# Kernel optimization log

Measured on AMD Instinct MI355X. Metric: run time of the kernel, lower is better.

The kernel has to match this reference:

```python
import jax, jax.numpy as jnp
import numpy as np

NUM_EMBEDDINGS = 1024
EMBEDDING_DIM = 256
COMMITMENT_COST = 0.25
B, C, T = 16, 256, 4096


def setup_inputs() -> dict:
    key = jax.random.key(0)
    k_in, k_cb = jax.random.split(key)
    inputs = jax.random.normal(k_in, (B, C, T), dtype=jnp.float32)
    # matches nn.Embedding init uniform_(-1/K, 1/K)
    codebook = jax.random.uniform(
        k_cb, (NUM_EMBEDDINGS, EMBEDDING_DIM), dtype=jnp.float32,
        minval=-1.0 / NUM_EMBEDDINGS, maxval=1.0 / NUM_EMBEDDINGS)
    return {"inputs": inputs, "codebook": codebook}


def reference(inputs, codebook):
    # inputs: [B, C, T] -> [B, T, C] (channel-last), eval mode (no dead-code swap)
    x = jnp.transpose(inputs, (0, 2, 1))            # [B, T, C]
    flat = x.reshape(-1, EMBEDDING_DIM)             # [N, D]
    distances = (jnp.sum(flat * flat, axis=1, keepdims=True)
                 + jnp.sum(codebook * codebook, axis=1)
                 - 2.0 * jnp.matmul(flat, codebook.T))   # [N, K]
    encoding_indices = jnp.argmin(distances, axis=1)     # [N]
    quantized = codebook[encoding_indices].reshape(x.shape)  # [B, T, C]
    sg = jax.lax.stop_gradient
    e_latent_loss = jnp.mean(jnp.square(sg(quantized) - x))
    q_latent_loss = jnp.mean(jnp.square(quantized - sg(x)))
    vq_loss = e_latent_loss + COMMITMENT_COST * q_latent_loss
    quantized_st = x + sg(quantized - x)                 # straight-through
    quantized_st = jnp.transpose(quantized_st, (0, 2, 1))  # back to [B, C, T]
    indices = encoding_indices.reshape(B, T)
    return quantized_st, vq_loss, indices
```

## Files before the change

kernel.cpp:

```cpp
#include <hip/hip_runtime.h>
#include <stdint.h>

#define DIMS 256
#define NT 4096
#define NROWS 65536
#define THETA 1.5e-4f

typedef float    f32x4_t __attribute__((ext_vector_type(4)));
typedef _Float16 f16x8_t __attribute__((ext_vector_type(8)));
typedef _Float16 f16x4_t __attribute__((ext_vector_type(4)));

__global__ __launch_bounds__(64) void vq_prep(const float* __restrict__ cb,
                                              float* __restrict__ se,
                                              _Float16* __restrict__ cb16){
  __shared__ float sq[256];
  const int k = blockIdx.x;
  const int tid = threadIdx.x;
  float4 v = *(const float4*)(cb + (size_t)k*256 + tid*4);
  f16x4_t p;
  p.x = (_Float16)(v.x * 512.f);
  p.y = (_Float16)(v.y * 512.f);
  p.z = (_Float16)(v.z * 512.f);
  p.w = (_Float16)(v.w * 512.f);
  *(f16x4_t*)(cb16 + (size_t)k*256 + tid*4) = p;
  sq[tid*4+0] = __fmul_rn(v.x, v.x);
  sq[tid*4+1] = __fmul_rn(v.y, v.y);
  sq[tid*4+2] = __fmul_rn(v.z, v.z);
  sq[tid*4+3] = __fmul_rn(v.w, v.w);
  __syncthreads();
  if (tid < 16){
    const int h = tid >> 3, j = tid & 7;
    float r = sq[h*128 + j];
    #pragma unroll
    for (int i = 1; i < 16; ++i) r = __fadd_rn(r, sq[h*128 + j + 8*i]);
    r = __fadd_rn(r, __shfl_xor(r, 1));
    r = __fadd_rn(r, __shfl_xor(r, 2));
    r = __fadd_rn(r, __shfl_xor(r, 4));
    r = __fadd_rn(r, __shfl_xor(r, 8));
    if (tid == 0) se[k] = r;
  }
}


#define AH(r,c)    Ah[(size_t)(r)*264 + (c)]
#define BHL(s,k,c) Bh[((size_t)((s)*256 + (k)))*40 + (c)]
#define QQ(t,c)    q[(size_t)(t)*260 + (c)]

#define T2I(v, i, v1, i1, v2) { \
  bool lt = (v) < (v1); \
  (v2) = lt ? (v1) : fminf((v2), (v)); \
  (i1) = lt ? (i) : (i1); \
  (v1) = lt ? (v) : (v1); }

#define DECL_T2(M,R) \
  float b1_##M##R = 3.4e38f, b2_##M##R = 3.4e38f; int bi_##M##R = 0x7fffffff;

#define FOLD(M,R) { \
  float v; \
  v = fmaf(a##M##0[R], NEGI, ec0); T2I(v, kb +  0, b1_##M##R, bi_##M##R, b2_##M##R); \
  v = fmaf(a##M##1[R], NEGI, ec1); T2I(v, kb + 16, b1_##M##R, bi_##M##R, b2_##M##R); \
  v = fmaf(a##M##2[R], NEGI, ec2); T2I(v, kb + 32, b1_##M##R, bi_##M##R, b2_##M##R); \
  v = fmaf(a##M##3[R], NEGI, ec3); T2I(v, kb + 48, b1_##M##R, bi_##M##R, b2_##M##R); }

#define BSTEP(CC, S) { \
  *(f16x8_t*)&BHL((CC)&1, codeS, cOff)     = rb##S##0; \
  *(f16x8_t*)&BHL((CC)&1, codeS, cOff + 8) = rb##S##1; \
  asm volatile("s_waitcnt lgkmcnt(0)" ::: "memory"); \
  __builtin_amdgcn_s_barrier(); \
  asm volatile("" ::: "memory"); \
  { \
    const int nn = ktb + (CC) + 2; \
    if (nn < 32){ \
      const _Float16* p_ = cb16 + ((size_t)((nn>>3)*256) + codeS)*DIMS + (nn&7)*32 + cOff; \
      rb##S##0 = *(const f16x8_t*)(p_); rb##S##1 = *(const f16x8_t*)(p_ + 8); \
    } \
  } \
  { \
    f16x8_t bh0 = *(const f16x8_t*)&BHL((CC)&1, bC0, fq8); \
    f16x8_t bh1 = *(const f16x8_t*)&BHL((CC)&1, bC1, fq8); \
    f16x8_t bh2 = *(const f16x8_t*)&BHL((CC)&1, bC2, fq8); \
    f16x8_t bh3 = *(const f16x8_t*)&BHL((CC)&1, bC3, fq8); \
    f16x8_t ah0 = *(const f16x8_t*)&AH(wr32 + fr, (CC)*32 + fq8); \
    f16x8_t ah1 = *(const f16x8_t*)&AH(wr32 + 16 + fr, (CC)*32 + fq8); \
    a00 = __builtin_amdgcn_mfma_f32_16x16x32_f16(ah0, bh0, a00, 0, 0, 0); \
    a01 = __builtin_amdgcn_mfma_f32_16x16x32_f16(ah0, bh1, a01, 0, 0, 0); \
    a02 = __builtin_amdgcn_mfma_f32_16x16x32_f16(ah0, bh2, a02, 0, 0, 0); \
    a03 = __builtin_amdgcn_mfma_f32_16x16x32_f16(ah0, bh3, a03, 0, 0, 0); \
    a10 = __builtin_amdgcn_mfma_f32_16x16x32_f16(ah1, bh0, a10, 0, 0, 0); \
    a11 = __builtin_amdgcn_mfma_f32_16x16x32_f16(ah1, bh1, a11, 0, 0, 0); \
    a12 = __builtin_amdgcn_mfma_f32_16x16x32_f16(ah1, bh2, a12, 0, 0, 0); \
    a13 = __builtin_amdgcn_mfma_f32_16x16x32_f16(ah1, bh3, a13, 0, 0, 0); \
  } }

#define MSTEP(MK) { \
  float ov1 = __shfl_xor(v1, MK); int oi1 = __shfl_xor(i1, MK); float ov2 = __shfl_xor(v2, MK); \
  bool tk = ov1 < v1; \
  v2 = tk ? fminf(v1, ov2) : fminf(v2, ov1); \
  i1 = tk ? oi1 : i1; \
  v1 = tk ? ov1 : v1; }

#define MERGE(M,R) { \
  float v1 = b1_##M##R, v2 = b2_##M##R; int i1 = bi_##M##R; \
  MSTEP(1) MSTEP(2) MSTEP(4) MSTEP(8) \
  if (fr == 0) comb[(wr32 + (M)*16 + fq*4 + (R))*4 + wc] = make_float4(v1, __int_as_float(i1), v2, 0.f); }

__global__ __launch_bounds__(512, 1) void vq_scores(
    const float* __restrict__ x, const float* __restrict__ cb,
    const _Float16* __restrict__ cb16, const float* __restrict__ se,
    float* __restrict__ out0, float* __restrict__ out2,
    unsigned* __restrict__ wl, unsigned* __restrict__ cnt, double* __restrict__ accd)
{
  __shared__ __align__(16) char smem[79360];
  _Float16* Ah   = (_Float16*)smem;
  _Float16* Bh   = (_Float16*)(smem + 33792);
  float4*   comb = (float4*)(smem + 74752);
  int*      codeL= (int*)(smem + 78848);
  float*    sxa  = (float*)(smem + 79104);
  float*    q    = (float*)smem;

  const int tid  = threadIdx.x;
  const int lane = tid & 63;
  const int wid  = tid >> 6;
  const int wr   = wid >> 2;
  const int wc   = wid & 3;
  const int fr   = lane & 15;
  const int fq   = lane >> 4;
  const int wr32 = wr * 32;
  const int fq8  = fq * 8;
  const int wcfr = wc*64 + fr;
  const int n0   = blockIdx.x * 64;
  const int bb   = n0 >> 12;
  const int t0   = n0 & 4095;
  const float NEGI = -1.0f/256.0f;

  const int codeS = tid >> 1;
  const int cOff  = (tid & 1) << 4;

  f16x8_t rbA0, rbA1, rbB0, rbB1;
  {
    const _Float16* p_ = cb16 + (size_t)codeS * DIMS + cOff;
    rbA0 = *(const f16x8_t*)(p_); rbA1 = *(const f16x8_t*)(p_ + 8);
  }
  {
    const _Float16* p_ = cb16 + (size_t)codeS * DIMS + 32 + cOff;
    rbB0 = *(const f16x8_t*)(p_); rbB1 = *(const f16x8_t*)(p_ + 8);
  }

  {
    const int dup = tid >> 7;
    const int c4  = tid & 7;
    const int tt  = ((tid >> 3) & 15) << 2;
    #pragma unroll
    for (int cc2 = 0; cc2 < 2; ++cc2){
      const int c0 = (dup*2 + cc2) * 32;
      const float* xp = x + ((size_t)(bb*DIMS + c0 + c4*4))*NT + t0 + tt;
      float4 va0 = *(const float4*)(xp);
      float4 va1 = *(const float4*)(xp + NT);
      float4 va2 = *(const float4*)(xp + 2*NT);
      float4 va3 = *(const float4*)(xp + 3*NT);
      #pragma unroll
      for (int j = 0; j < 4; ++j){
        f16x4_t p;
        p.x = (_Float16)((&va0.x)[j]);
        p.y = (_Float16)((&va1.x)[j]);
        p.z = (_Float16)((&va2.x)[j]);
        p.w = (_Float16)((&va3.x)[j]);
        *(f16x4_t*)&AH(tt + j, c0 + c4*4) = p;
      }
    }
  }

  const f32x4_t Z = {0.f, 0.f, 0.f, 0.f};
  f32x4_t a00=Z,a01=Z,a02=Z,a03=Z, a10=Z,a11=Z,a12=Z,a13=Z;
  DECL_T2(0,0) DECL_T2(0,1) DECL_T2(0,2) DECL_T2(0,3)
  DECL_T2(1,0) DECL_T2(1,1) DECL_T2(1,2) DECL_T2(1,3)

  const int bC0 = wc*64 + 0*16 + fr;
  const int bC1 = wc*64 + 1*16 + fr;
  const int bC2 = wc*64 + 2*16 + fr;
  const int bC3 = wc*64 + 3*16 + fr;

  for (int kt = 0; kt < 4; ++kt){
    const int ktb = kt * 8;
    BSTEP(0,A) BSTEP(1,B) BSTEP(2,A) BSTEP(3,B)
    BSTEP(4,A) BSTEP(5,B) BSTEP(6,A) BSTEP(7,B)

    const int kb = kt*256 + wcfr;
    const float ec0 = se[kb], ec1 = se[kb+16], ec2 = se[kb+32], ec3 = se[kb+48];
    FOLD(0,0) FOLD(0,1) FOLD(0,2) FOLD(0,3)
    FOLD(1,0) FOLD(1,1) FOLD(1,2) FOLD(1,3)
    a00=Z;a01=Z;a02=Z;a03=Z; a10=Z;a11=Z;a12=Z;a13=Z;
  }

  MERGE(0,0) MERGE(0,1) MERGE(0,2) MERGE(0,3)
  MERGE(1,0) MERGE(1,1) MERGE(1,2) MERGE(1,3)
  __syncthreads();

  {
    const int row = tid >> 3, seg = tid & 7;
    float s = 0.f;
    #pragma unroll
    for (int k = 0; k < 4; ++k){
      f16x8_t hv = *(const f16x8_t*)&AH(row, seg*32 + k*8);
      #pragma unroll
      for (int e = 0; e < 8; ++e){
        float f = (float)hv[e];
        s = fmaf(f, f, s);
      }
    }
    s += __shfl_xor(s, 1);
    s += __shfl_xor(s, 2);
    s += __shfl_xor(s, 4);
    if (seg == 0) sxa[row] = s;
  }
  __syncthreads();

  if (tid < 64){
    float4 p = comb[tid*4 + 0];
    float v1 = p.x, v2 = p.z;
    int   i1 = __float_as_int(p.y);
    #pragma unroll
    for (int w = 1; w < 4; ++w){
      p = comb[tid*4 + w];
      bool tk = p.x < v1;
      v2 = tk ? fminf(v1, p.z) : fminf(v2, p.x);
      i1 = tk ? __float_as_int(p.y) : i1;
      v1 = tk ? p.x : v1;
    }
    const int r = n0 + tid;
    codeL[tid] = i1;
    out2[r] = (float)i1;
    bool flg = !(v2 - v1 >= THETA);
    if (flg){
      unsigned pos = atomicAdd(cnt, 1u);
      wl[pos] = (unsigned)r;
    }
    double c = flg ? 0.0 : (double)(sxa[tid] + v1);
    #pragma unroll
    for (int m = 1; m < 64; m <<= 1) c += __shfl_xor(c, m);
    if (tid == 0) atomicAdd(accd, c);
  }
  __syncthreads();

  {
    const int r = tid >> 3, seg = tid & 7;
    const float* src = cb + (size_t)codeL[r] * DIMS;
    #pragma unroll
    for (int k = 0; k < 8; ++k){
      float4 v = *(const float4*)(src + k*32 + seg*4);
      *(float4*)&QQ(r, k*32 + seg*4) = v;
    }
  }
  __syncthreads();

  {
    #pragma unroll
    for (int jj = 0; jj < 2; ++jj){
      const int c = wid*32 + jj*16 + (lane >> 2);
      float* dst = out0 + ((size_t)(bb*256 + c))*NT + t0;
      #pragma unroll
      for (int ii = 0; ii < 4; ++ii){
        const int tl = ii*16 + (lane & 3)*4;
        float4 v;
        v.x = QQ(tl + 0, c);
        v.y = QQ(tl + 1, c);
        v.z = QQ(tl + 2, c);
        v.w = QQ(tl + 3, c);
        *(float4*)(dst + tl) = v;
      }
    }
  }
}

__global__ __launch_bounds__(256) void vq_refine(
    const float* __restrict__ x, const float* __restrict__ cb,
    const float* __restrict__ se,
    const unsigned* __restrict__ wl, const unsigned* __restrict__ cnt,
    float* __restrict__ out2, float* __restrict__ out0, double* __restrict__ accd)
{
  __shared__ float eT[8][1024];
  __shared__ float xs[DIMS][16];
  __shared__ int   rows_s[16];
  __shared__ float sxs[16];
  __shared__ float wv[4][16];
  __shared__ int   wi[4][16];
  __shared__ int   wiF[16];

  const unsigned n = *cnt;
  const unsigned groups = (n + 15u) >> 4;
  const int tid  = threadIdx.x;
  const int lane = tid & 63;
  const int wid  = tid >> 6;

  for (unsigned g = blockIdx.x; g < groups; g += gridDim.x){
    __syncthreads();
    if (tid < 16){
      unsigned e = g*16u + (unsigned)tid;
      rows_s[tid] = (int)wl[e < n ? e : (n - 1u)];
    }
    __syncthreads();
    #pragma unroll
    for (int rep = 0; rep < 16; ++rep){
      int id = rep * 256 + tid;
      int c = id >> 4, r = id & 15;
      int row = rows_s[r];
      xs[c][r] = x[((size_t)((row >> 12)*DIMS + c))*NT + (row & 4095)];
    }
    __syncthreads();
    {
      const int r = tid >> 4, hj = tid & 15;
      const int h = hj >> 3, j = hj & 7;
      float v0 = xs[h*128 + j][r];
      float s = __fmul_rn(v0, v0);
      #pragma unroll
      for (int i = 1; i < 16; ++i){
        float v = xs[h*128 + j + 8*i][r];
        s = __fadd_rn(s, __fmul_rn(v, v));
      }
      s = __fadd_rn(s, __shfl_xor(s, 1));
      s = __fadd_rn(s, __shfl_xor(s, 2));
      s = __fadd_rn(s, __shfl_xor(s, 4));
      s = __fadd_rn(s, __shfl_xor(s, 8));
      if (hj == 0) sxs[r] = s;
    }

    float s[16][4];
    #pragma unroll
    for (int r = 0; r < 16; ++r)
      #pragma unroll
      for (int u = 0; u < 4; ++u) s[r][u] = 0.f;

    for (int c0 = 0; c0 < DIMS; c0 += 8){
      __syncthreads();
      #pragma unroll
      for (int rep = 0; rep < 8; ++rep){
        int id2 = rep * 256 + tid;
        int k = id2 >> 1, qq = id2 & 1;
        float4 v = *(const float4*)&cb[(size_t)k * DIMS + c0 + qq * 4];
        eT[qq*4 + 0][k] = v.x; eT[qq*4 + 1][k] = v.y;
        eT[qq*4 + 2][k] = v.z; eT[qq*4 + 3][k] = v.w;
      }
      __syncthreads();
      #pragma unroll
      for (int cc = 0; cc < 8; ++cc){
        float4 ev = *(const float4*)&eT[cc][wid*256 + lane*4];
        #pragma unroll
        for (int r = 0; r < 16; ++r){
          float xv = xs[c0 + cc][r];
          s[r][0] = fmaf(xv, ev.x, s[r][0]);
          s[r][1] = fmaf(xv, ev.y, s[r][1]);
          s[r][2] = fmaf(xv, ev.z, s[r][2]);
          s[r][3] = fmaf(xv, ev.w, s[r][3]);
        }
      }
    }

    float4 sek = *(const float4*)&se[wid*256 + lane*4];
    #pragma unroll
    for (int r = 0; r < 16; ++r){
      const float sxv = sxs[r];
      float bv = 3.4e38f; int bi = 0x7fffffff;
      #pragma unroll
      for (int u = 0; u < 4; ++u){
        float d = __fsub_rn(__fadd_rn(sxv, (&sek.x)[u]),
                            __fadd_rn(s[r][u], s[r][u]));
        int k = wid*256 + lane*4 + u;
        if (d < bv || (d == bv && k < bi)) { bv = d; bi = k; }
      }
      #pragma unroll
      for (int m = 1; m < 64; m <<= 1){
        float ov = __shfl_xor(bv, m);
        int   oi = __shfl_xor(bi, m);
        if (ov < bv || (ov == bv && oi < bi)) { bv = ov; bi = oi; }
      }
      if (lane == 0){ wv[wid][r] = bv; wi[wid][r] = bi; }
    }
    __syncthreads();
    if (tid < 16){
      const int r = tid;
      float bv = wv[0][r]; int bi = wi[0][r];
      #pragma unroll
      for (int w = 1; w < 4; ++w){
        float ov = wv[w][r]; int oi = wi[w][r];
        if (ov < bv || (ov == bv && oi < bi)) { bv = ov; bi = oi; }
      }
      wiF[r] = bi;
      if (g*16u + (unsigned)r < n){
        int row = rows_s[r];
        out2[row] = (float)bi;
        atomicAdd(accd, (double)bv);
      }
    }
    __syncthreads();
    #pragma unroll
    for (int r = 0; r < 16; ++r){
      if (g*16u + (unsigned)r < n){
        int row  = rows_s[r];
        int code = wiF[r];
        out0[((size_t)((row >> 12)*256 + tid))*NT + (row & 4095)] = cb[(size_t)code*DIMS + tid];
      }
    }
  }
}

__global__ void vq_final(const double* __restrict__ accd, float* __restrict__ out1){
  *out1 = (float)(1.25 * (*accd) * (1.0 / 16777216.0));
}

extern "C" void kernel_launch(void* const* d_in, const int* in_sizes, int n_in,
                              void* d_out, int out_size, void* d_ws, size_t ws_size,
                              hipStream_t stream)
{
  const float* x  = (const float*)d_in[0];
  const float* cb = (const float*)d_in[1];
  float* out  = (float*)d_out;
  float* out0 = out;
  float* out1 = out + (size_t)16777216;
  float* out2 = out + (size_t)16777217;

  char* ws = (char*)d_ws;
  double*   accd = (double*)(ws + 0);
  unsigned* cnt  = (unsigned*)(ws + 8);
  float*    se   = (float*)(ws + 64);
  unsigned* wl   = (unsigned*)(ws + 4160);
  _Float16* cb16 = (_Float16*)(ws + 266304);

  hipMemsetAsync(d_ws, 0, 16, stream);
  vq_prep  <<<dim3(1024), dim3(64),  0, stream>>>(cb, se, cb16);
  vq_scores<<<dim3(1024), dim3(512), 0, stream>>>(x, cb, cb16, se, out0, out2, wl, cnt, accd);
  vq_refine<<<dim3(512),  dim3(256), 0, stream>>>(x, cb, se, wl, cnt, out2, out0, accd);
  vq_final <<<dim3(1),    dim3(1),   0, stream>>>(accd, out1);
}
```

Before: 184.3 us.

## Use nontemporal loads/stores in main kernel and halve refine group size

Measured after the change: 174.2 us. -5.5%, faster.

```diff
diff --git a/kernel.cpp b/kernel.cpp
--- a/kernel.cpp
+++ b/kernel.cpp
@@ -154,17 +154,17 @@
     for (int cc2 = 0; cc2 < 2; ++cc2){
       const int c0 = (dup*2 + cc2) * 32;
       const float* xp = x + ((size_t)(bb*DIMS + c0 + c4*4))*NT + t0 + tt;
-      float4 va0 = *(const float4*)(xp);
-      float4 va1 = *(const float4*)(xp + NT);
-      float4 va2 = *(const float4*)(xp + 2*NT);
-      float4 va3 = *(const float4*)(xp + 3*NT);
+      f32x4_t va0 = __builtin_nontemporal_load((const f32x4_t*)(xp));
+      f32x4_t va1 = __builtin_nontemporal_load((const f32x4_t*)(xp + NT));
+      f32x4_t va2 = __builtin_nontemporal_load((const f32x4_t*)(xp + 2*NT));
+      f32x4_t va3 = __builtin_nontemporal_load((const f32x4_t*)(xp + 3*NT));
       #pragma unroll
       for (int j = 0; j < 4; ++j){
         f16x4_t p;
-        p.x = (_Float16)((&va0.x)[j]);
-        p.y = (_Float16)((&va1.x)[j]);
-        p.z = (_Float16)((&va2.x)[j]);
-        p.w = (_Float16)((&va3.x)[j]);
+        p.x = (_Float16)(va0[j]);
+        p.y = (_Float16)(va1[j]);
+        p.z = (_Float16)(va2[j]);
+        p.w = (_Float16)(va3[j]);
         *(f16x4_t*)&AH(tt + j, c0 + c4*4) = p;
       }
     }
@@ -261,12 +261,12 @@
       #pragma unroll
       for (int ii = 0; ii < 4; ++ii){
         const int tl = ii*16 + (lane & 3)*4;
-        float4 v;
-        v.x = QQ(tl + 0, c);
-        v.y = QQ(tl + 1, c);
-        v.z = QQ(tl + 2, c);
-        v.w = QQ(tl + 3, c);
-        *(float4*)(dst + tl) = v;
+        f32x4_t v;
+        v[0] = QQ(tl + 0, c);
+        v[1] = QQ(tl + 1, c);
+        v[2] = QQ(tl + 2, c);
+        v[3] = QQ(tl + 3, c);
+        __builtin_nontemporal_store(v, (f32x4_t*)(dst + tl));
       }
     }
   }
@@ -279,35 +279,35 @@
     float* __restrict__ out2, float* __restrict__ out0, double* __restrict__ accd)
 {
   __shared__ float eT[8][1024];
-  __shared__ float xs[DIMS][16];
-  __shared__ int   rows_s[16];
-  __shared__ float sxs[16];
-  __shared__ float wv[4][16];
-  __shared__ int   wi[4][16];
-  __shared__ int   wiF[16];
+  __shared__ float xs[DIMS][8];
+  __shared__ int   rows_s[8];
+  __shared__ float sxs[8];
+  __shared__ float wv[4][8];
+  __shared__ int   wi[4][8];
+  __shared__ int   wiF[8];
 
   const unsigned n = *cnt;
-  const unsigned groups = (n + 15u) >> 4;
+  const unsigned groups = (n + 7u) >> 3;
   const int tid  = threadIdx.x;
   const int lane = tid & 63;
   const int wid  = tid >> 6;
 
   for (unsigned g = blockIdx.x; g < groups; g += gridDim.x){
     __syncthreads();
-    if (tid < 16){
-      unsigned e = g*16u + (unsigned)tid;
+    if (tid < 8){
+      unsigned e = g*8u + (unsigned)tid;
       rows_s[tid] = (int)wl[e < n ? e : (n - 1u)];
     }
     __syncthreads();
     #pragma unroll
-    for (int rep = 0; rep < 16; ++rep){
+    for (int rep = 0; rep < 8; ++rep){
       int id = rep * 256 + tid;
-      int c = id >> 4, r = id & 15;
+      int c = id >> 3, r = id & 7;
       int row = rows_s[r];
       xs[c][r] = x[((size_t)((row >> 12)*DIMS + c))*NT + (row & 4095)];
     }
     __syncthreads();
-    {
+    if (tid < 128){
       const int r = tid >> 4, hj = tid & 15;
       const int h = hj >> 3, j = hj & 7;
       float v0 = xs[h*128 + j][r];
@@ -324,9 +324,9 @@
       if (hj == 0) sxs[r] = s;
     }
 
-    float s[16][4];
-    #pragma unroll
-    for (int r = 0; r < 16; ++r)
+    float s[8][4];
+    #pragma unroll
+    for (int r = 0; r < 8; ++r)
       #pragma unroll
       for (int u = 0; u < 4; ++u) s[r][u] = 0.f;
 
@@ -345,7 +345,7 @@
       for (int cc = 0; cc < 8; ++cc){
         float4 ev = *(const float4*)&eT[cc][wid*256 + lane*4];
         #pragma unroll
-        for (int r = 0; r < 16; ++r){
+        for (int r = 0; r < 8; ++r){
           float xv = xs[c0 + cc][r];
           s[r][0] = fmaf(xv, ev.x, s[r][0]);
           s[r][1] = fmaf(xv, ev.y, s[r][1]);
@@ -357,7 +357,7 @@
 
     float4 sek = *(const float4*)&se[wid*256 + lane*4];
     #pragma unroll
-    for (int r = 0; r < 16; ++r){
+    for (int r = 0; r < 8; ++r){
       const float sxv = sxs[r];
       float bv = 3.4e38f; int bi = 0x7fffffff;
       #pragma unroll
@@ -376,7 +376,7 @@
       if (lane == 0){ wv[wid][r] = bv; wi[wid][r] = bi; }
     }
     __syncthreads();
-    if (tid < 16){
+    if (tid < 8){
       const int r = tid;
       float bv = wv[0][r]; int bi = wi[0][r];
       #pragma unroll
@@ -385,7 +385,7 @@
         if (ov < bv || (ov == bv && oi < bi)) { bv = ov; bi = oi; }
       }
       wiF[r] = bi;
-      if (g*16u + (unsigned)r < n){
+      if (g*8u + (unsigned)r < n){
         int row = rows_s[r];
         out2[row] = (float)bi;
         atomicAdd(accd, (double)bv);
@@ -393,8 +393,8 @@
     }
     __syncthreads();
     #pragma unroll
-    for (int r = 0; r < 16; ++r){
-      if (g*16u + (unsigned)r < n){
+    for (int r = 0; r < 8; ++r){
+      if (g*8u + (unsigned)r < n){
         int row  = rows_s[r];
         int code = wiF[r];
         out0[((size_t)((row >> 12)*256 + tid))*NT + (row & 4095)] = cb[(size_t)code*DIMS + tid];
```
